# Optimization experiments

Measured on AMD Instinct MI355X. Metric: run time of the kernel, lower is better.

## Reference

```python
import jax, jax.numpy as jnp
import numpy as np

B, T, N_EMBD = 8, 2048, 512
N_HEAD = 4
EPS = 1e-5
NEG_INF = -1e9


def setup_inputs() -> dict:
    key = jax.random.key(0)
    ks = jax.random.split(key, 10)
    x = jax.random.normal(ks[0], (B, T, N_EMBD), dtype=jnp.float32)
    # relative-position index map [t, t] into a (2t-1)-entry boolean mask table
    pos_emb = jax.random.randint(ks[1], (T, T), 0, 2 * T - 1)
    ln_w = jax.random.normal(ks[2], (N_EMBD,), dtype=jnp.float32) * 0.02 + 1.0
    ln_b = jax.random.normal(ks[3], (N_EMBD,), dtype=jnp.float32) * 0.02
    aff_w = jax.random.normal(ks[4], (N_EMBD,), dtype=jnp.float32) * 0.02 + 1.0
    aff_b = jax.random.normal(ks[5], (N_EMBD,), dtype=jnp.float32) * 0.02
    W_qkv = jax.random.normal(ks[6], (N_EMBD, 3 * N_EMBD), dtype=jnp.float32) * (N_EMBD ** -0.5)
    # boolean lookup table; True = position visible (mostly visible)
    mask_table = jax.random.uniform(ks[7], (2 * T - 1,)) > 0.2
    W_proj = jax.random.normal(ks[8], (N_EMBD, N_EMBD), dtype=jnp.float32) * (N_EMBD ** -0.5)
    return {
        "x": x, "pos_emb": pos_emb, "ln_w": ln_w, "ln_b": ln_b,
        "aff_w": aff_w, "aff_b": aff_b, "W_qkv": W_qkv,
        "mask_table": mask_table, "W_proj": W_proj,
    }


def reference(x, pos_emb, ln_w, ln_b, aff_w, aff_b, W_qkv, mask_table, W_proj):
    b, t, n = x.shape
    hd = n // N_HEAD
    # LayerNorm (mean subtract, rms normalize, affine)
    x = x - jnp.mean(x, axis=-1, keepdims=True)
    x = x * jax.lax.rsqrt(jnp.mean(x * x, axis=-1, keepdims=True) + EPS)
    x = x * ln_w + ln_b
    # extra affine (onnx initializers 7/8) then fused QKV projection
    x = x * aff_w + aff_b
    qkv = x @ W_qkv                       # [b, t, 3n]
    q, k, v = jnp.split(qkv, 3, axis=2)
    q = q.reshape(b, t, N_HEAD, hd).transpose(0, 2, 1, 3)  # [b, h, t, hd]
    k = k.reshape(b, t, N_HEAD, hd).transpose(0, 2, 1, 3)
    v = v.reshape(b, t, N_HEAD, hd).transpose(0, 2, 1, 3)
    scale = 1.0 / np.sqrt(hd).astype(np.float32)
    scores = jnp.einsum('bhqd,bhkd->bhqk', q, k) * scale   # [b, h, t, t]
    # gather-based relative-position mask: True = attend, False = mask out
    mask = mask_table[pos_emb]                             # [t, t] bool
    scores = jnp.where(mask, scores, NEG_INF)
    attn = jax.nn.softmax(scores, axis=-1)
    out = jnp.einsum('bhqk,bhkd->bhqd', attn, v)           # [b, h, t, hd]
    out = out.transpose(0, 2, 1, 3).reshape(b, t, n)
    return out @ W_proj
```

## Files before the change

kernel.cpp:

```cpp
#include <hip/hip_runtime.h>
#include <hip/hip_bf16.h>

#define T_SEQ 2048
#define NEMBD 512
#define NHEAD 4
#define HDIM  128
#define BATCH 8
#define MROWS (BATCH * T_SEQ)
#define QSCALE 0.12751744534f

typedef __attribute__((ext_vector_type(8))) short short8;
typedef __attribute__((ext_vector_type(4))) short short4v;
typedef __attribute__((ext_vector_type(4))) float f32x4;

static __device__ __forceinline__ float bf2f(unsigned short h) {
  return __uint_as_float(((unsigned int)h) << 16);
}
static __device__ __forceinline__ short f2bs(float f) {
  unsigned int u = __float_as_uint(f);
  unsigned int r = (u + 0x7FFFu + ((u >> 16) & 1u)) >> 16;
  return (short)r;
}
static __device__ __forceinline__ unsigned int pk2(float a, float b) {
  __hip_bfloat162 h = __float22bfloat162_rn(make_float2(a, b));
  return *reinterpret_cast<unsigned int*>(&h);
}
static __device__ __forceinline__ int mask_at(const void* mt, int fmt, int idx) {
  if (fmt == 0) return ((const int*)mt)[idx] != 0;
  if (fmt == 1) return ((const unsigned char*)mt)[idx] != 0;
  if (fmt == 2) return ((const float*)mt)[idx] != 0.0f;
  return ((const unsigned short*)mt)[idx] != 0;
}
static __device__ __forceinline__ int pos_at(const int* pos, int i64, size_t idx) {
  return i64 ? pos[idx * 2] : pos[idx];
}
static __device__ __forceinline__ void gload16(const void* g, void* l) {
  __builtin_amdgcn_global_load_lds((const __attribute__((address_space(1))) void*)g,
                                   (__attribute__((address_space(3))) void*)l,
                                   16, 0, 0);
}

__global__ __launch_bounds__(256) void detect_kernel(
    const unsigned int* __restrict__ mt, const unsigned int* __restrict__ posw,
    int* __restrict__ flags)
{
  __shared__ int s01, sf, sbf, szero;
  const int t = threadIdx.x;
  if (t == 0) { s01 = 1; sf = 1; sbf = 1; szero = 0; }
  __syncthreads();
  int a01 = 1, af = 1, ab = 1, zc = 0;
  for (int i = t; i < 1023; i += 256) {
    const unsigned int v = mt[i];
    if (v > 1u) a01 = 0;
    const float f = __uint_as_float(v);
    if (!(f == 0.0f || f == 1.0f)) af = 0;
    const unsigned int lo = v & 0xFFFFu, hi = v >> 16;
    if (!((lo == 0u || lo == 0x3F80u) && (hi == 0u || hi == 0x3F80u))) ab = 0;
  }
  for (int i = t; i < 512; i += 256) if (posw[2 * i + 1] == 0u) zc++;
  if (!a01) atomicAnd(&s01, 0);
  if (!af)  atomicAnd(&sf, 0);
  if (!ab)  atomicAnd(&sbf, 0);
  if (zc)   atomicAdd(&szero, zc);
  __syncthreads();
  if (t == 0) {
    flags[0] = s01 ? 0 : (sf ? 2 : (sbf ? 3 : 1));
    flags[2] = (szero > 500) ? 1 : 0;
  }
}

__global__ __launch_bounds__(256) void pack_mask_kernel(
    const int* __restrict__ pos, const void* __restrict__ mt,
    const int* __restrict__ flags, unsigned int* __restrict__ mp)
{
  const int idx = blockIdx.x * 256 + threadIdx.x;
  const int fmt = flags[0];
  const int i64 = flags[2];
  const int q = idx >> 6;
  const int wrd = idx & 63;
  const size_t base = (size_t)q * T_SEQ + wrd * 32;
  unsigned int bits = 0;
  #pragma unroll 4
  for (int j = 0; j < 32; ++j)
    bits |= (mask_at(mt, fmt, pos_at(pos, i64, base + j)) ? 1u : 0u) << j;
  mp[idx] = bits;
}

__global__ __launch_bounds__(256) void vecprep_kernel(
    const float* __restrict__ lnw, const float* __restrict__ lnb,
    const float* __restrict__ afw, const float* __restrict__ afb,
    float* __restrict__ effw, float* __restrict__ effb)
{
  const int c = blockIdx.x * 256 + threadIdx.x;
  if (c >= NEMBD) return;
  effw[c] = lnw[c] * afw[c];
  effb[c] = lnb[c] * afw[c] + afb[c];
}

__global__ __launch_bounds__(256) void wconv_kernel(
    const float* __restrict__ W, short* __restrict__ Wt, int N)
{
  const int idx = blockIdx.x * 256 + threadIdx.x;
  const int n = idx >> 9;
  const int k = idx & 511;
  if (n >= N) return;
  Wt[idx] = f2bs(W[(size_t)k * N + n]);
}

__global__ __launch_bounds__(64) void ln_kernel(
    const float* __restrict__ x, const float* __restrict__ effw, const float* __restrict__ effb,
    short* __restrict__ xp)
{
  const int row = blockIdx.x;
  const int tid = threadIdx.x;
  const float4* p = (const float4*)(x + (size_t)row * NEMBD + tid * 8);
  const float4 a0 = p[0], a1 = p[1];
  float f[8] = {a0.x, a0.y, a0.z, a0.w, a1.x, a1.y, a1.z, a1.w};
  float s = 0.f, s2 = 0.f;
  #pragma unroll
  for (int j = 0; j < 8; ++j) { s += f[j]; s2 += f[j] * f[j]; }
  #pragma unroll
  for (int off = 1; off < 64; off <<= 1) {
    s  += __shfl_xor(s, off);
    s2 += __shfl_xor(s2, off);
  }
  const float mean = s * (1.0f / NEMBD);
  const float rstd = rsqrtf(s2 * (1.0f / NEMBD) - mean * mean + 1e-5f);
  const float4* wp = (const float4*)(effw + tid * 8);
  const float4* bp = (const float4*)(effb + tid * 8);
  const float4 w0 = wp[0], w1 = wp[1], b0 = bp[0], b1 = bp[1];
  short8 ob;
  ob[0] = f2bs((f[0] - mean) * rstd * w0.x + b0.x);
  ob[1] = f2bs((f[1] - mean) * rstd * w0.y + b0.y);
  ob[2] = f2bs((f[2] - mean) * rstd * w0.z + b0.z);
  ob[3] = f2bs((f[3] - mean) * rstd * w0.w + b0.w);
  ob[4] = f2bs((f[4] - mean) * rstd * w1.x + b1.x);
  ob[5] = f2bs((f[5] - mean) * rstd * w1.y + b1.y);
  ob[6] = f2bs((f[6] - mean) * rstd * w1.z + b1.z);
  ob[7] = f2bs((f[7] - mean) * rstd * w1.w + b1.w);
  *((short8*)(xp + (size_t)row * NEMBD + tid * 8)) = ob;
}

template<int MODE>
__global__ __launch_bounds__(256) void gemm_kernel(
    const short* __restrict__ A, const short* __restrict__ Bt,
    void* __restrict__ out0, short* __restrict__ Kp, short* __restrict__ Vt)
{
  __shared__ alignas(16) short Atile[128 * 64];
  __shared__ alignas(16) short Btile[128 * 64];
  const int tid = threadIdx.x;
  const int l = tid & 63;
  const int w = tid >> 6;
  const int m0 = blockIdx.x * 128;
  const int n0 = blockIdx.y * 128;
  const int w_r = w >> 1, w_c = w & 1;
  const int lr = l & 15, lg = l >> 4;
  f32x4 acc[4][4] = {};

  for (int kt = 0; kt < 512; kt += 64) {
    #pragma unroll
    for (int i = 0; i < 4; ++i) {
      const int c = i * 256 + tid;
      const int row = c >> 3, col8 = c & 7;
      gload16(A  + (size_t)(m0 + row) * 512 + kt + col8 * 8, Atile + (i * 256 + w * 64) * 8);
      gload16(Bt + (size_t)(n0 + row) * 512 + kt + col8 * 8, Btile + (i * 256 + w * 64) * 8);
    }
    __syncthreads();
    #pragma unroll
    for (int kk = 0; kk < 2; ++kk) {
      short8 af[4], bfm[4];
      #pragma unroll
      for (int m = 0; m < 4; ++m)
        af[m] = *(const short8*)&Atile[(w_r * 64 + m * 16 + lr) * 64 + kk * 32 + lg * 8];
      #pragma unroll
      for (int n = 0; n < 4; ++n)
        bfm[n] = *(const short8*)&Btile[(w_c * 64 + n * 16 + lr) * 64 + kk * 32 + lg * 8];
      #pragma unroll
      for (int m = 0; m < 4; ++m)
        #pragma unroll
        for (int n = 0; n < 4; ++n)
          acc[m][n] = __builtin_amdgcn_mfma_f32_16x16x32_bf16(af[m], bfm[n], acc[m][n], 0, 0, 0);
    }
    __syncthreads();
  }

  if (MODE == 1) {
    float* out = (float*)out0;
    #pragma unroll
    for (int m = 0; m < 4; ++m)
      #pragma unroll
      for (int n = 0; n < 4; ++n)
        #pragma unroll
        for (int r = 0; r < 4; ++r) {
          const int gm = m0 + w_r * 64 + m * 16 + lg * 4 + r;
          const int gn = n0 + w_c * 64 + n * 16 + lr;
          out[(size_t)gm * NEMBD + gn] = acc[m][n][r];
        }
  } else {
    const int which = n0 >> 9;
    const int h = (n0 >> 7) & 3;
    short* Qp = (short*)out0;
    #pragma unroll
    for (int m = 0; m < 4; ++m)
      #pragma unroll
      for (int n = 0; n < 4; ++n)
        #pragma unroll
        for (int r = 0; r < 4; ++r) {
          const int gm = m0 + w_r * 64 + m * 16 + lg * 4 + r;
          const int b = gm >> 11, t = gm & 2047;
          const int d = w_c * 64 + n * 16 + lr;
          const size_t bh = (size_t)((b << 2) | h);
          const float v = acc[m][n][r];
          if (which == 0)      Qp[(bh * T_SEQ + t) * HDIM + d] = f2bs(v * QSCALE);
          else if (which == 1) Kp[(bh * T_SEQ + t) * HDIM + d] = f2bs(v);
          else                 Vt[(bh * HDIM + d) * T_SEQ + t] = f2bs(v);
        }
  }
}

__global__ __launch_bounds__(256, 4) void attn_kernel(
    const short* __restrict__ Q, const short* __restrict__ Kp, const short* __restrict__ Vt,
    const unsigned int* __restrict__ maskP, short* __restrict__ O)
{
  __shared__ alignas(16) short Kt[2][32 * 128];
  __shared__ alignas(16) short Vs[2][128 * 32];
  __shared__ alignas(16) short Pw[4][16 * 40];
  const int tid = threadIdx.x;
  const int l = tid & 63;
  const int w = tid >> 6;
  const int lr = l & 15, lg = l >> 4;
  const int s7 = lr & 7;
  const int vkey = (lr >> 1) & 3;
  const int swz = ((blockIdx.x & 7) << 7) | (blockIdx.x >> 3);
  const int bh = swz >> 5;
  const int q0 = (swz & 31) * 64 + w * 16;
  const short* Qb = Q  + (size_t)bh * T_SEQ * HDIM;
  const short* Kb = Kp + (size_t)bh * T_SEQ * HDIM;
  const short* Vb = Vt + (size_t)bh * HDIM * T_SEQ;

  #define STAGE(b, kti) do {                                                        \
    const int kt_ = (kti) * 32;                                                     \
    _Pragma("unroll")                                                               \
    for (int i = 0; i < 2; ++i) {                                                   \
      const int r = i * 16 + (tid >> 4);                                            \
      gload16(Kb + (size_t)(kt_ + r) * HDIM + ((tid & 15) ^ (r & 7)) * 8,           \
              (char*)&Kt[b][0] + i * 4096 + w * 1024);                              \
    }                                                                               \
    _Pragma("unroll")                                                               \
    for (int i = 0; i < 2; ++i) {                                                   \
      const int r = i * 64 + (tid >> 2);                                            \
      gload16(Vb + (size_t)r * T_SEQ + kt_ + ((tid & 3) ^ ((r >> 1) & 3)) * 8,      \
              (char*)&Vs[b][0] + i * 4096 + w * 1024);                              \
    }                                                                               \
  } while (0)

  short8 aq[4];
  #pragma unroll
  for (int kk = 0; kk < 4; ++kk)
    aq[kk] = *(const short8*)(Qb + (size_t)(q0 + lr) * HDIM + kk * 32 + lg * 8);

  float lsum = 0.f;
  f32x4 acc[8] = {};
  const size_t mrow = (size_t)(q0 + lr) * 64;

  STAGE(0, 0);
  __syncthreads();
  int cur = 0;
  for (int kti = 0; kti < 64; ++kti) {
    if (kti + 1 < 64) STAGE(cur ^ 1, kti + 1);
    const unsigned int mq = maskP[mrow + kti];
    f32x4 sn[2];
    __builtin_amdgcn_s_setprio(1);
    #pragma unroll
    for (int n = 0; n < 2; ++n) {
      f32x4 s = {};
      #pragma unroll
      for (int kk = 0; kk < 4; ++kk) {
        const short8 bk = *(const short8*)((char*)&Kt[cur][0]
            + (n * 16 + lr) * 256 + ((kk * 4 + lg) ^ s7) * 16);
        s = __builtin_amdgcn_mfma_f32_16x16x32_bf16(bk, aq[kk], s, 0, 0, 0);
      }
      sn[n] = s;
    }
    __builtin_amdgcn_s_setprio(0);
    #pragma unroll
    for (int n = 0; n < 2; ++n) {
      const int base = n * 16 + lg * 4;
      const float p0 = __builtin_amdgcn_exp2f(((mq >> (base + 0)) & 1) ? sn[n][0] : -1e9f);
      const float p1 = __builtin_amdgcn_exp2f(((mq >> (base + 1)) & 1) ? sn[n][1] : -1e9f);
      const float p2 = __builtin_amdgcn_exp2f(((mq >> (base + 2)) & 1) ? sn[n][2] : -1e9f);
      const float p3 = __builtin_amdgcn_exp2f(((mq >> (base + 3)) & 1) ? sn[n][3] : -1e9f);
      lsum += (p0 + p1) + (p2 + p3);
      union { short4v s4; unsigned int u[2]; } pwv;
      pwv.u[0] = pk2(p0, p1);
      pwv.u[1] = pk2(p2, p3);
      *(short4v*)&Pw[w][lr * 40 + base] = pwv.s4;
    }
    const short8 pa = *(const short8*)&Pw[w][lr * 40 + lg * 8];
    __builtin_amdgcn_s_setprio(1);
    #pragma unroll
    for (int nn = 0; nn < 8; ++nn) {
      const short8 bv = *(const short8*)((char*)&Vs[cur][0]
          + (nn * 16 + lr) * 64 + (lg ^ vkey) * 16);
      acc[nn] = __builtin_amdgcn_mfma_f32_16x16x32_bf16(pa, bv, acc[nn], 0, 0, 0);
    }
    __builtin_amdgcn_s_setprio(0);
    __syncthreads();
    cur ^= 1;
  }
  #undef STAGE

  float s = lsum;
  s += __shfl_xor(s, 16);
  s += __shfl_xor(s, 32);
  const float rin = 1.0f / s;
  float rin4[4];
  #pragma unroll
  for (int r = 0; r < 4; ++r) rin4[r] = __shfl(rin, lg * 4 + r);
  const int b = bh >> 2, h = bh & 3;
  #pragma unroll
  for (int nn = 0; nn < 8; ++nn) {
    const int d = nn * 16 + lr;
    #pragma unroll
    for (int r = 0; r < 4; ++r) {
      const int qg = q0 + lg * 4 + r;
      O[((size_t)b * T_SEQ + qg) * NEMBD + h * HDIM + d] = f2bs(acc[nn][r] * rin4[r]);
    }
  }
}

__global__ __launch_bounds__(256) void fill_kernel(float* __restrict__ out, float v, size_t n) {
  for (size_t i = blockIdx.x * 256 + threadIdx.x; i < n; i += (size_t)gridDim.x * 256)
    out[i] = v;
}

extern "C" void kernel_launch(void* const* d_in, const int* in_sizes, int n_in,
                              void* d_out, int out_size, void* d_ws, size_t ws_size,
                              hipStream_t stream)
{
  const float* x     = (const float*)d_in[0];
  const int*   pos   = (const int*)d_in[1];
  const float* lnw   = (const float*)d_in[2];
  const float* lnb   = (const float*)d_in[3];
  const float* afw   = (const float*)d_in[4];
  const float* afb   = (const float*)d_in[5];
  const float* Wqkv  = (const float*)d_in[6];
  const void*  mtab  = d_in[7];
  const float* Wproj = (const float*)d_in[8];

  size_t off = 0;
  char* ws = (char*)d_ws;
  int* flags = (int*)(ws + off);                   off += 256;
  float* effw = (float*)(ws + off);                off += 2048;
  float* effb = (float*)(ws + off);                off += 2048;
  unsigned int* maskP = (unsigned int*)(ws + off); off += (size_t)T_SEQ * 64 * 4;
  short* Xp  = (short*)(ws + off);                 off += (size_t)MROWS * NEMBD * 2;
  short* WqT = (short*)(ws + off);                 off += (size_t)3 * NEMBD * NEMBD * 2;
  short* WpT = (short*)(ws + off);                 off += (size_t)NEMBD * NEMBD * 2;
  short* Qb  = (short*)(ws + off);                 off += (size_t)BATCH * NHEAD * T_SEQ * HDIM * 2;
  short* Kb  = (short*)(ws + off);                 off += (size_t)BATCH * NHEAD * T_SEQ * HDIM * 2;
  short* Vt  = (short*)(ws + off);                 off += (size_t)BATCH * NHEAD * T_SEQ * HDIM * 2;
  short* Ob  = Xp;

  if (ws_size < off) {
    fill_kernel<<<256, 256, 0, stream>>>((float*)d_out, (float)(ws_size >> 20), (size_t)out_size);
    return;
  }

  detect_kernel<<<1, 256, 0, stream>>>((const unsigned int*)mtab, (const unsigned int*)pos, flags);
  pack_mask_kernel<<<(T_SEQ * (T_SEQ / 32)) / 256, 256, 0, stream>>>(pos, mtab, flags, maskP);
  vecprep_kernel<<<2, 256, 0, stream>>>(lnw, lnb, afw, afb, effw, effb);
  wconv_kernel<<<3072, 256, 0, stream>>>(Wqkv, WqT, 1536);
  wconv_kernel<<<1024, 256, 0, stream>>>(Wproj, WpT, 512);
  ln_kernel<<<MROWS, 64, 0, stream>>>(x, effw, effb, Xp);
  dim3 g0(128, 12);
  gemm_kernel<0><<<g0, 256, 0, stream>>>(Xp, WqT, (void*)Qb, Kb, Vt);
  attn_kernel<<<1024, 256, 0, stream>>>(Qb, Kb, Vt, maskP, Ob);
  dim3 g1(128, 4);
  gemm_kernel<1><<<g1, 256, 0, stream>>>(Ob, WpT, d_out, nullptr, nullptr);
}
```

Baseline: 234.6 us.

## Widen attention blocks to 8 waves sharing K/V tiles and merge weight conversions

Attention blocks grow from 4 to 8 waves (128 query rows per block, 512 blocks). Each staged 32-key K/V tile is now shared by twice as many query rows, which halves the global K/V traffic per query and gives each thread one load instead of two. The two weight-conversion launches are also merged into one kernel. The larger blocks may reduce occupancy and scheduling flexibility, and launch_bounds(512,4) may constrain registers.

```diff
diff --git a/kernel.cpp b/kernel.cpp
--- a/kernel.cpp
+++ b/kernel.cpp
@@ -97,14 +97,19 @@
   effb[c] = lnb[c] * afw[c] + afb[c];
 }
 
-__global__ __launch_bounds__(256) void wconv_kernel(
-    const float* __restrict__ W, short* __restrict__ Wt, int N)
+__global__ __launch_bounds__(256) void wconv2_kernel(
+    const float* __restrict__ Wq, const float* __restrict__ Wp,
+    short* __restrict__ WqT, short* __restrict__ WpT)
 {
   const int idx = blockIdx.x * 256 + threadIdx.x;
-  const int n = idx >> 9;
-  const int k = idx & 511;
-  if (n >= N) return;
-  Wt[idx] = f2bs(W[(size_t)k * N + n]);
+  if (idx < 1536 * 512) {
+    const int n = idx >> 9, k = idx & 511;
+    WqT[idx] = f2bs(Wq[(size_t)k * 1536 + n]);
+  } else {
+    const int j = idx - 1536 * 512;
+    const int n = j >> 9, k = j & 511;
+    WpT[j] = f2bs(Wp[(size_t)k * 512 + n]);
+  }
 }
 
 __global__ __launch_bounds__(64) void ln_kernel(
@@ -218,40 +223,34 @@
   }
 }
 
-__global__ __launch_bounds__(256, 4) void attn_kernel(
+__global__ __launch_bounds__(512, 4) void attn_kernel(
     const short* __restrict__ Q, const short* __restrict__ Kp, const short* __restrict__ Vt,
     const unsigned int* __restrict__ maskP, short* __restrict__ O)
 {
   __shared__ alignas(16) short Kt[2][32 * 128];
   __shared__ alignas(16) short Vs[2][128 * 32];
-  __shared__ alignas(16) short Pw[4][16 * 40];
+  __shared__ alignas(16) short Pw[8][16 * 40];
   const int tid = threadIdx.x;
   const int l = tid & 63;
   const int w = tid >> 6;
   const int lr = l & 15, lg = l >> 4;
   const int s7 = lr & 7;
   const int vkey = (lr >> 1) & 3;
-  const int swz = ((blockIdx.x & 7) << 7) | (blockIdx.x >> 3);
-  const int bh = swz >> 5;
-  const int q0 = (swz & 31) * 64 + w * 16;
+  const int swz = ((blockIdx.x & 7) << 6) | (blockIdx.x >> 3);
+  const int bh = swz >> 4;
+  const int q0 = (swz & 15) * 128 + w * 16;
   const short* Qb = Q  + (size_t)bh * T_SEQ * HDIM;
   const short* Kb = Kp + (size_t)bh * T_SEQ * HDIM;
   const short* Vb = Vt + (size_t)bh * HDIM * T_SEQ;
 
+  const int kr = tid >> 4, kc = tid & 15;
+  const int vr = tid >> 2, vc = tid & 3;
   #define STAGE(b, kti) do {                                                        \
     const int kt_ = (kti) * 32;                                                     \
-    _Pragma("unroll")                                                               \
-    for (int i = 0; i < 2; ++i) {                                                   \
-      const int r = i * 16 + (tid >> 4);                                            \
-      gload16(Kb + (size_t)(kt_ + r) * HDIM + ((tid & 15) ^ (r & 7)) * 8,           \
-              (char*)&Kt[b][0] + i * 4096 + w * 1024);                              \
-    }                                                                               \
-    _Pragma("unroll")                                                               \
-    for (int i = 0; i < 2; ++i) {                                                   \
-      const int r = i * 64 + (tid >> 2);                                            \
-      gload16(Vb + (size_t)r * T_SEQ + kt_ + ((tid & 3) ^ ((r >> 1) & 3)) * 8,      \
-              (char*)&Vs[b][0] + i * 4096 + w * 1024);                              \
-    }                                                                               \
+    gload16(Kb + (size_t)(kt_ + kr) * HDIM + (kc ^ (kr & 7)) * 8,                   \
+            (char*)&Kt[b][0] + w * 1024);                                           \
+    gload16(Vb + (size_t)vr * T_SEQ + kt_ + (vc ^ ((vr >> 1) & 3)) * 8,             \
+            (char*)&Vs[b][0] + w * 1024);                                           \
   } while (0)
 
   short8 aq[4];
@@ -370,12 +369,11 @@
   detect_kernel<<<1, 256, 0, stream>>>((const unsigned int*)mtab, (const unsigned int*)pos, flags);
   pack_mask_kernel<<<(T_SEQ * (T_SEQ / 32)) / 256, 256, 0, stream>>>(pos, mtab, flags, maskP);
   vecprep_kernel<<<2, 256, 0, stream>>>(lnw, lnb, afw, afb, effw, effb);
-  wconv_kernel<<<3072, 256, 0, stream>>>(Wqkv, WqT, 1536);
-  wconv_kernel<<<1024, 256, 0, stream>>>(Wproj, WpT, 512);
+  wconv2_kernel<<<(4 * NEMBD * NEMBD) / 256, 256, 0, stream>>>(Wqkv, Wproj, WqT, WpT);
   ln_kernel<<<MROWS, 64, 0, stream>>>(x, effw, effb, Xp);
   dim3 g0(128, 12);
   gemm_kernel<0><<<g0, 256, 0, stream>>>(Xp, WqT, (void*)Qb, Kb, Vt);
-  attn_kernel<<<1024, 256, 0, stream>>>(Qb, Kb, Vt, maskP, Ob);
+  attn_kernel<<<512, 512, 0, stream>>>(Qb, Kb, Vt, maskP, Ob);
   dim3 g1(128, 4);
   gemm_kernel<1><<<g1, 256, 0, stream>>>(Ob, WpT, d_out, nullptr, nullptr);
 }
```

After: 219.9 us. 6.2% less time.
